# Performance work log

Hardware: AMD Instinct MI355X
Metric: run time of the kernel (lower is better)

The kernel has to match this reference:

```python
import jax, jax.numpy as jnp
import numpy as np

B, N, U = 8, 4096, 128
AVG_DEG = 32.0  # expected neighbors per node


def setup_inputs() -> dict:
    key = jax.random.key(0)
    k1, k2, k3 = jax.random.split(key, 3)
    x = jax.random.normal(k1, (B, N, U), dtype=jnp.float32)
    # sparse-ish binary adjacency, ~AVG_DEG neighbors per node
    adj = (jax.random.uniform(k2, (B, N, N)) < (AVG_DEG / N)).astype(jnp.float32)
    W = jax.random.normal(k3, (U, U), dtype=jnp.float32) * 0.05
    b = jnp.zeros((U,), dtype=jnp.float32)
    return {"x": x, "adj": adj, "W": W, "b": b}


def reference(x, adj, W, b):
    # adjacency is stop_gradient'd in the original module
    adj = jax.lax.stop_gradient(adj)

    def step(h):
        # batched SpMM (dense here): [B,N,N] @ [B,N,U] -> [B,N,U]
        hn = jnp.einsum('bij,bjd->bid', adj, h)
        # aggregate_mode='graph_conv': no degree normalization
        return jax.nn.swish(hn @ W + b)

    # eval mode: K_l = 2 message-passing iterations
    return step(step(x))
```

## Files before the change

kernel.cpp:

```cpp
#include <hip/hip_runtime.h>
#include <math.h>

#define BB 8
#define NN 4096
#define UU 128
#define CAP 128

typedef float f4_t __attribute__((ext_vector_type(4)));

__global__ __launch_bounds__(256) void build_idx_kernel(
    const float* __restrict__ adj,
    unsigned short* __restrict__ idx,
    int* __restrict__ deg)
{
    const int row = blockIdx.x;
    const f4_t* arow = (const f4_t*)(adj + (size_t)row * NN);

    __shared__ int cnt;
    __shared__ unsigned short sidx[CAP];
    if (threadIdx.x == 0) cnt = 0;
    __syncthreads();

    #pragma unroll
    for (int it = 0; it < 4; ++it) {
        const int v = it * 256 + threadIdx.x;
        const f4_t a = __builtin_nontemporal_load(arow + v);
        const int jb = v * 4;
        if (a[0] != 0.f) { int p = atomicAdd(&cnt, 1); if (p < CAP) sidx[p] = (unsigned short)(jb + 0); }
        if (a[1] != 0.f) { int p = atomicAdd(&cnt, 1); if (p < CAP) sidx[p] = (unsigned short)(jb + 1); }
        if (a[2] != 0.f) { int p = atomicAdd(&cnt, 1); if (p < CAP) sidx[p] = (unsigned short)(jb + 2); }
        if (a[3] != 0.f) { int p = atomicAdd(&cnt, 1); if (p < CAP) sidx[p] = (unsigned short)(jb + 3); }
    }
    __syncthreads();

    int d = cnt; if (d > CAP) d = CAP;
    if (threadIdx.x == 0) deg[row] = d;
    for (int t = (int)threadIdx.x; t < d; t += 256)
        idx[(size_t)row * CAP + t] = sidx[t];
}

__global__ __launch_bounds__(256) void aggregate_kernel(
    const float* __restrict__ h,
    const unsigned short* __restrict__ idx,
    const int* __restrict__ deg,
    float* __restrict__ hn)
{
    __shared__ unsigned short sidx[8 * CAP];
    __shared__ int sdeg[8];

    const int row0 = blockIdx.x * 8;

    {
        const uint4* g = (const uint4*)(idx + (size_t)row0 * CAP);
        if (threadIdx.x < 128) ((uint4*)sidx)[threadIdx.x] = g[threadIdx.x];
        if (threadIdx.x < 8)   sdeg[threadIdx.x] = deg[row0 + threadIdx.x];
    }
    __syncthreads();

    const int rg   = threadIdx.x >> 5;
    const int lane = threadIdx.x & 31;
    const int row  = row0 + rg;
    const int b    = row >> 12;

    const float4* hb = (const float4*)(h + (size_t)b * NN * UU);
    const unsigned short* my = &sidx[rg * CAP];
    const int d = sdeg[rg];

    float4 a0 = make_float4(0.f,0.f,0.f,0.f), a1 = a0, a2 = a0, a3 = a0;
    int n = 0;
    for (; n + 8 <= d; n += 8) {
        const int j0 = my[n+0], j1 = my[n+1], j2 = my[n+2], j3 = my[n+3];
        const int j4 = my[n+4], j5 = my[n+5], j6 = my[n+6], j7 = my[n+7];
        const float4 v0 = hb[j0 * 32 + lane];
        const float4 v1 = hb[j1 * 32 + lane];
        const float4 v2 = hb[j2 * 32 + lane];
        const float4 v3 = hb[j3 * 32 + lane];
        const float4 v4 = hb[j4 * 32 + lane];
        const float4 v5 = hb[j5 * 32 + lane];
        const float4 v6 = hb[j6 * 32 + lane];
        const float4 v7 = hb[j7 * 32 + lane];
        a0.x += v0.x + v4.x; a0.y += v0.y + v4.y; a0.z += v0.z + v4.z; a0.w += v0.w + v4.w;
        a1.x += v1.x + v5.x; a1.y += v1.y + v5.y; a1.z += v1.z + v5.z; a1.w += v1.w + v5.w;
        a2.x += v2.x + v6.x; a2.y += v2.y + v6.y; a2.z += v2.z + v6.z; a2.w += v2.w + v6.w;
        a3.x += v3.x + v7.x; a3.y += v3.y + v7.y; a3.z += v3.z + v7.z; a3.w += v3.w + v7.w;
    }
    for (; n < d; ++n) {
        const int j = my[n];
        const float4 v = hb[j * 32 + lane];
        a0.x += v.x; a0.y += v.y; a0.z += v.z; a0.w += v.w;
    }
    float4 acc;
    acc.x = (a0.x + a1.x) + (a2.x + a3.x);
    acc.y = (a0.y + a1.y) + (a2.y + a3.y);
    acc.z = (a0.z + a1.z) + (a2.z + a3.z);
    acc.w = (a0.w + a1.w) + (a2.w + a3.w);
    ((float4*)hn)[(size_t)row * 32 + lane] = acc;
}

__global__ __launch_bounds__(256) void gemm_swish_kernel(
    const float* __restrict__ hn,
    const float* __restrict__ Wm,
    const float* __restrict__ bias,
    float* __restrict__ out)
{
    __shared__ float s[64 * UU];

    const int row0 = blockIdx.x * 64;
    const float4* src = (const float4*)(hn + (size_t)row0 * UU);
    float4* d4 = (float4*)s;
    #pragma unroll
    for (int i = 0; i < 8; ++i)
        d4[i * 256 + threadIdx.x] = src[i * 256 + threadIdx.x];
    __syncthreads();

    const int cg = threadIdx.x & 31;
    const int r0 = (threadIdx.x >> 5) * 8;

    float acc[8][4];
    #pragma unroll
    for (int r = 0; r < 8; ++r)
        #pragma unroll
        for (int c = 0; c < 4; ++c) acc[r][c] = 0.f;

    const float4* W4 = (const float4*)Wm;
    #pragma unroll 4
    for (int k = 0; k < UU; k += 4) {
        const float4 w0 = W4[(k + 0) * 32 + cg];
        const float4 w1 = W4[(k + 1) * 32 + cg];
        const float4 w2 = W4[(k + 2) * 32 + cg];
        const float4 w3 = W4[(k + 3) * 32 + cg];
        #pragma unroll
        for (int r = 0; r < 8; ++r) {
            const float4 sv = *(const float4*)&s[(r0 + r) * UU + k];
            acc[r][0] += sv.x * w0.x + sv.y * w1.x + sv.z * w2.x + sv.w * w3.x;
            acc[r][1] += sv.x * w0.y + sv.y * w1.y + sv.z * w2.y + sv.w * w3.y;
            acc[r][2] += sv.x * w0.z + sv.y * w1.z + sv.z * w2.z + sv.w * w3.z;
            acc[r][3] += sv.x * w0.w + sv.y * w1.w + sv.z * w2.w + sv.w * w3.w;
        }
    }

    const float4 bb = ((const float4*)bias)[cg];
    #pragma unroll
    for (int r = 0; r < 8; ++r) {
        const int row = row0 + r0 + r;
        float4 o;
        float v;
        v = acc[r][0] + bb.x; o.x = v / (1.f + expf(-v));
        v = acc[r][1] + bb.y; o.y = v / (1.f + expf(-v));
        v = acc[r][2] + bb.z; o.z = v / (1.f + expf(-v));
        v = acc[r][3] + bb.w; o.w = v / (1.f + expf(-v));
        ((float4*)out)[(size_t)row * 32 + cg] = o;
    }
}

extern "C" void kernel_launch(void* const* d_in, const int* in_sizes, int n_in,
                              void* d_out, int out_size, void* d_ws, size_t ws_size,
                              hipStream_t stream)
{
    const float* x    = (const float*)d_in[0];
    const float* adj  = (const float*)d_in[1];
    const float* Wm   = (const float*)d_in[2];
    const float* bias = (const float*)d_in[3];
    float* out = (float*)d_out;

    const int R = BB * NN;

    char* ws = (char*)d_ws;
    unsigned short* idx = (unsigned short*)ws;
    int* deg = (int*)(ws + (size_t)R * CAP * sizeof(unsigned short));
    float* hn = (float*)(ws + (size_t)R * CAP * sizeof(unsigned short)
                            + (size_t)R * sizeof(int));

    build_idx_kernel<<<R, 256, 0, stream>>>(adj, idx, deg);

    aggregate_kernel<<<R / 8, 256, 0, stream>>>(x, idx, deg, hn);
    gemm_swish_kernel<<<R / 64, 256, 0, stream>>>(hn, Wm, bias, out);

    aggregate_kernel<<<R / 8, 256, 0, stream>>>(out, idx, deg, hn);
    gemm_swish_kernel<<<R / 64, 256, 0, stream>>>(hn, Wm, bias, out);
}
```

Before: 783.6 us.

## Fuse adjacency scan with first aggregation using wave-ballot compaction

Merges the index-building kernel and the first neighbor aggregation into one kernel where each 64-lane wavefront scans one adjacency row. It replaces per-element shared-memory atomics with ballot/popcount stream compaction, and then immediately gathers x rows from the in-shared indices. This removes one launch and the idx/deg round-trip for the first layer and avoids atomic contention. The ballot approach keeps neighbor order deterministic, but each wave now handles a full 16KB row with serialized ballot steps.

```diff
diff --git a/kernel.cpp b/kernel.cpp
--- a/kernel.cpp
+++ b/kernel.cpp
@@ -7,36 +7,79 @@
 #define CAP 128
 
 typedef float f4_t __attribute__((ext_vector_type(4)));
-
-__global__ __launch_bounds__(256) void build_idx_kernel(
+typedef float f2_t __attribute__((ext_vector_type(2)));
+
+__global__ __launch_bounds__(256) void scan_agg_kernel(
     const float* __restrict__ adj,
+    const float* __restrict__ x,
     unsigned short* __restrict__ idx,
-    int* __restrict__ deg)
-{
-    const int row = blockIdx.x;
+    int* __restrict__ deg,
+    float* __restrict__ hn)
+{
+    __shared__ unsigned short sidx[4][CAP];
+
+    const int w    = threadIdx.x >> 6;
+    const int lane = threadIdx.x & 63;
+    const int row  = blockIdx.x * 4 + w;
+    const int b    = row >> 12;
     const f4_t* arow = (const f4_t*)(adj + (size_t)row * NN);
 
-    __shared__ int cnt;
-    __shared__ unsigned short sidx[CAP];
-    if (threadIdx.x == 0) cnt = 0;
+    int cnt = 0;
+    #pragma unroll
+    for (int it = 0; it < 16; it += 4) {
+        f4_t buf[4];
+        #pragma unroll
+        for (int j = 0; j < 4; ++j)
+            buf[j] = __builtin_nontemporal_load(arow + (it + j) * 64 + lane);
+        #pragma unroll
+        for (int j = 0; j < 4; ++j) {
+            const int jb = ((it + j) * 64 + lane) * 4;
+            #pragma unroll
+            for (int c = 0; c < 4; ++c) {
+                const bool nz = (buf[j][c] != 0.f);
+                const unsigned long long m = __ballot(nz);
+                if (nz) {
+                    const int p = cnt + (int)__popcll(m & ((1ull << lane) - 1ull));
+                    if (p < CAP) sidx[w][p] = (unsigned short)(jb + c);
+                }
+                cnt += (int)__popcll(m);
+            }
+        }
+    }
+    if (cnt > CAP) cnt = CAP;
+    if (lane == 0) deg[row] = cnt;
     __syncthreads();
 
-    #pragma unroll
-    for (int it = 0; it < 4; ++it) {
-        const int v = it * 256 + threadIdx.x;
-        const f4_t a = __builtin_nontemporal_load(arow + v);
-        const int jb = v * 4;
-        if (a[0] != 0.f) { int p = atomicAdd(&cnt, 1); if (p < CAP) sidx[p] = (unsigned short)(jb + 0); }
-        if (a[1] != 0.f) { int p = atomicAdd(&cnt, 1); if (p < CAP) sidx[p] = (unsigned short)(jb + 1); }
-        if (a[2] != 0.f) { int p = atomicAdd(&cnt, 1); if (p < CAP) sidx[p] = (unsigned short)(jb + 2); }
-        if (a[3] != 0.f) { int p = atomicAdd(&cnt, 1); if (p < CAP) sidx[p] = (unsigned short)(jb + 3); }
-    }
-    __syncthreads();
-
-    int d = cnt; if (d > CAP) d = CAP;
-    if (threadIdx.x == 0) deg[row] = d;
-    for (int t = (int)threadIdx.x; t < d; t += 256)
-        idx[(size_t)row * CAP + t] = sidx[t];
+    for (int t = lane; t < cnt; t += 64)
+        idx[(size_t)row * CAP + t] = sidx[w][t];
+
+    const f2_t* hb = (const f2_t*)(x + (size_t)b * NN * UU);
+    const unsigned short* my = sidx[w];
+
+    f2_t a0 = (f2_t)0.f, a1 = (f2_t)0.f, a2 = (f2_t)0.f, a3 = (f2_t)0.f;
+    int n = 0;
+    for (; n + 8 <= cnt; n += 8) {
+        const int j0 = my[n+0], j1 = my[n+1], j2 = my[n+2], j3 = my[n+3];
+        const int j4 = my[n+4], j5 = my[n+5], j6 = my[n+6], j7 = my[n+7];
+        const f2_t v0 = hb[j0 * 64 + lane];
+        const f2_t v1 = hb[j1 * 64 + lane];
+        const f2_t v2 = hb[j2 * 64 + lane];
+        const f2_t v3 = hb[j3 * 64 + lane];
+        const f2_t v4 = hb[j4 * 64 + lane];
+        const f2_t v5 = hb[j5 * 64 + lane];
+        const f2_t v6 = hb[j6 * 64 + lane];
+        const f2_t v7 = hb[j7 * 64 + lane];
+        a0 += v0 + v4;
+        a1 += v1 + v5;
+        a2 += v2 + v6;
+        a3 += v3 + v7;
+    }
+    for (; n < cnt; ++n) {
+        const int j = my[n];
+        a0 += hb[j * 64 + lane];
+    }
+    const f2_t acc = (a0 + a1) + (a2 + a3);
+    ((f2_t*)hn)[(size_t)row * 64 + lane] = acc;
 }
 
 __global__ __launch_bounds__(256) void aggregate_kernel(
@@ -49,7 +92,6 @@
     __shared__ int sdeg[8];
 
     const int row0 = blockIdx.x * 8;
-
     {
         const uint4* g = (const uint4*)(idx + (size_t)row0 * CAP);
         if (threadIdx.x < 128) ((uint4*)sidx)[threadIdx.x] = g[threadIdx.x];
@@ -66,7 +108,7 @@
     const unsigned short* my = &sidx[rg * CAP];
     const int d = sdeg[rg];
 
-    float4 a0 = make_float4(0.f,0.f,0.f,0.f), a1 = a0, a2 = a0, a3 = a0;
+    f4_t a0 = (f4_t)0.f, a1 = (f4_t)0.f, a2 = (f4_t)0.f, a3 = (f4_t)0.f;
     int n = 0;
     for (; n + 8 <= d; n += 8) {
         const int j0 = my[n+0], j1 = my[n+1], j2 = my[n+2], j3 = my[n+3];
@@ -79,22 +121,18 @@
         const float4 v5 = hb[j5 * 32 + lane];
         const float4 v6 = hb[j6 * 32 + lane];
         const float4 v7 = hb[j7 * 32 + lane];
-        a0.x += v0.x + v4.x; a0.y += v0.y + v4.y; a0.z += v0.z + v4.z; a0.w += v0.w + v4.w;
-        a1.x += v1.x + v5.x; a1.y += v1.y + v5.y; a1.z += v1.z + v5.z; a1.w += v1.w + v5.w;
-        a2.x += v2.x + v6.x; a2.y += v2.y + v6.y; a2.z += v2.z + v6.z; a2.w += v2.w + v6.w;
-        a3.x += v3.x + v7.x; a3.y += v3.y + v7.y; a3.z += v3.z + v7.z; a3.w += v3.w + v7.w;
+        a0[0] += v0.x + v4.x; a0[1] += v0.y + v4.y; a0[2] += v0.z + v4.z; a0[3] += v0.w + v4.w;
+        a1[0] += v1.x + v5.x; a1[1] += v1.y + v5.y; a1[2] += v1.z + v5.z; a1[3] += v1.w + v5.w;
+        a2[0] += v2.x + v6.x; a2[1] += v2.y + v6.y; a2[2] += v2.z + v6.z; a2[3] += v2.w + v6.w;
+        a3[0] += v3.x + v7.x; a3[1] += v3.y + v7.y; a3[2] += v3.z + v7.z; a3[3] += v3.w + v7.w;
     }
     for (; n < d; ++n) {
         const int j = my[n];
         const float4 v = hb[j * 32 + lane];
-        a0.x += v.x; a0.y += v.y; a0.z += v.z; a0.w += v.w;
-    }
-    float4 acc;
-    acc.x = (a0.x + a1.x) + (a2.x + a3.x);
-    acc.y = (a0.y + a1.y) + (a2.y + a3.y);
-    acc.z = (a0.z + a1.z) + (a2.z + a3.z);
-    acc.w = (a0.w + a1.w) + (a2.w + a3.w);
-    ((float4*)hn)[(size_t)row * 32 + lane] = acc;
+        a0[0] += v.x; a0[1] += v.y; a0[2] += v.z; a0[3] += v.w;
+    }
+    f4_t acc = (a0 + a1) + (a2 + a3);
+    ((f4_t*)hn)[(size_t)row * 32 + lane] = acc;
 }
 
 __global__ __launch_bounds__(256) void gemm_swish_kernel(
@@ -131,11 +169,11 @@
         const float4 w3 = W4[(k + 3) * 32 + cg];
         #pragma unroll
         for (int r = 0; r < 8; ++r) {
-            const float4 sv = *(const float4*)&s[(r0 + r) * UU + k];
-            acc[r][0] += sv.x * w0.x + sv.y * w1.x + sv.z * w2.x + sv.w * w3.x;
-            acc[r][1] += sv.x * w0.y + sv.y * w1.y + sv.z * w2.y + sv.w * w3.y;
-            acc[r][2] += sv.x * w0.z + sv.y * w1.z + sv.z * w2.z + sv.w * w3.z;
-            acc[r][3] += sv.x * w0.w + sv.y * w1.w + sv.z * w2.w + sv.w * w3.w;
+            const f4_t sv = *(const f4_t*)&s[(r0 + r) * UU + k];
+            acc[r][0] += sv[0] * w0.x + sv[1] * w1.x + sv[2] * w2.x + sv[3] * w3.x;
+            acc[r][1] += sv[0] * w0.y + sv[1] * w1.y + sv[2] * w2.y + sv[3] * w3.y;
+            acc[r][2] += sv[0] * w0.z + sv[1] * w1.z + sv[2] * w2.z + sv[3] * w3.z;
+            acc[r][3] += sv[0] * w0.w + sv[1] * w1.w + sv[2] * w2.w + sv[3] * w3.w;
         }
     }
 
@@ -143,8 +181,7 @@
     #pragma unroll
     for (int r = 0; r < 8; ++r) {
         const int row = row0 + r0 + r;
-        float4 o;
-        float v;
+        float4 o; float v;
         v = acc[r][0] + bb.x; o.x = v / (1.f + expf(-v));
         v = acc[r][1] + bb.y; o.y = v / (1.f + expf(-v));
         v = acc[r][2] + bb.z; o.z = v / (1.f + expf(-v));
@@ -171,11 +208,11 @@
     float* hn = (float*)(ws + (size_t)R * CAP * sizeof(unsigned short)
                             + (size_t)R * sizeof(int));
 
-    build_idx_kernel<<<R, 256, 0, stream>>>(adj, idx, deg);
-
-    aggregate_kernel<<<R / 8, 256, 0, stream>>>(x, idx, deg, hn);
+    scan_agg_kernel<<<R / 4, 256, 0, stream>>>(adj, x, idx, deg, hn);
+
     gemm_swish_kernel<<<R / 64, 256, 0, stream>>>(hn, Wm, bias, out);
 
     aggregate_kernel<<<R / 8, 256, 0, stream>>>(out, idx, deg, hn);
+
     gemm_swish_kernel<<<R / 64, 256, 0, stream>>>(hn, Wm, bias, out);
 }
```

Measured after the change: 785.6 us. No clear change (+0.2%).
